# Kernel tuning notes

Measured on AMD Instinct MI355X. Metric: run time of the kernel, lower is better.

Reference implementation:

```python
import jax, jax.numpy as jnp
import numpy as np

N = 50000        # nodes
E = 800000       # edges (before self-loops)
DIM = 96         # model dim
HEADS = 4
HEAD_DIM = DIM // HEADS  # 24
SLOPE = 0.2      # GATConv default negative_slope
EPS = 1e-5       # LayerNorm eps


def setup_inputs() -> dict:
    key = jax.random.key(0)
    ks = jax.random.split(key, 10)
    s = 0.1
    return {
        "x": jax.random.normal(ks[0], (N, DIM), jnp.float32),
        "edge_index": jax.random.randint(ks[1], (2, E), 0, N, dtype=jnp.int64),
        "W": (jax.random.normal(ks[2], (DIM, HEADS * HEAD_DIM), jnp.float32) * s),
        "att_src": (jax.random.normal(ks[3], (HEADS, HEAD_DIM), jnp.float32) * s),
        "att_dst": (jax.random.normal(ks[4], (HEADS, HEAD_DIM), jnp.float32) * s),
        "gat_bias": jnp.zeros((DIM,), jnp.float32),
        "proj_W": (jax.random.normal(ks[5], (DIM, DIM), jnp.float32) * s),
        "proj_b": jnp.zeros((DIM,), jnp.float32),
        "ln_g": jnp.ones((DIM,), jnp.float32),
        "ln_b": jnp.zeros((DIM,), jnp.float32),
    }


def _gat_layer(x, edge_index, W, att_src, att_dst, gat_bias, proj_W, proj_b, ln_g, ln_b):
    # add self-loops (PyG GATConv default add_self_loops=True)
    loop = jnp.arange(N, dtype=edge_index.dtype)
    src = jnp.concatenate([edge_index[0], loop])  # [E+N] message sources j
    dst = jnp.concatenate([edge_index[1], loop])  # [E+N] message targets i

    # shared linear transform, split into heads: [N, H, D]
    h = (x @ W).reshape(N, HEADS, HEAD_DIM)
    a_src = jnp.einsum('nhd,hd->nh', h, att_src)  # [N, H]
    a_dst = jnp.einsum('nhd,hd->nh', h, att_dst)  # [N, H]

    # per-edge attention logits, leaky relu
    e = jax.nn.leaky_relu(a_src[src] + a_dst[dst], SLOPE)  # [E+N, H]

    # segment softmax over incoming edges of each destination node
    m = jax.ops.segment_max(e, dst, num_segments=N)        # [N, H]
    e = jnp.exp(e - m[dst])
    denom = jax.ops.segment_sum(e, dst, num_segments=N)    # [N, H] (>0: self-loops)
    alpha = e / denom[dst]                                 # [E+N, H]

    # weighted scatter-aggregate of source features
    out = jax.ops.segment_sum(alpha[:, :, None] * h[src], dst, num_segments=N)
    out = out.reshape(N, HEADS * HEAD_DIM) + gat_bias      # concat heads + bias

    # trailing proj + residual + LayerNorm (dropout inactive at eval)
    proj = out @ proj_W.T + proj_b
    z = x + proj
    mu = jnp.mean(z, axis=-1, keepdims=True)
    var = jnp.mean((z - mu) ** 2, axis=-1, keepdims=True)
    return ln_g * (z - mu) / jnp.sqrt(var + EPS) + ln_b


def reference(x, edge_index, W, att_src, att_dst, gat_bias, proj_W, proj_b, ln_g, ln_b):
    return _gat_layer(x, edge_index, W, att_src, att_dst, gat_bias, proj_W, proj_b, ln_g, ln_b)
```

## Files before the change

### kernel.cpp

```cpp
#include <hip/hip_runtime.h>
#include <hip/hip_bf16.h>
#include <math.h>

#define N_NODES 50000
#define N_EDGES 800000
#define DIM 96
#define HEADS 4
#define HEAD_DIM 24
#define SLOPE 0.2f
#define LN_EPS 1e-5f

#define CH 2048
#define NCH ((N_EDGES + CH - 1) / CH)
#define NB2 ((N_NODES + 255) / 256)

#define NGRP (N_NODES / 16)
#define GRID_MM 784
#define HLP 100

typedef __attribute__((ext_vector_type(8))) short bf16x8;
typedef __attribute__((ext_vector_type(4))) float f32x4;

__device__ __forceinline__ unsigned short f2bf(float f) {
    unsigned u = __float_as_uint(f);
    u += 0x7FFFu + ((u >> 16) & 1u);
    return (unsigned short)(u >> 16);
}
__device__ __forceinline__ float bf2f(unsigned short v) {
    return __uint_as_float(((unsigned)v) << 16);
}
__device__ __forceinline__ unsigned pack2bf(float a, float b) {
    return (unsigned)f2bf(a) | ((unsigned)f2bf(b) << 16);
}

__global__ __launch_bounds__(256) void k_sortA(
    const int* __restrict__ ei, int* __restrict__ cnt,
    const float* __restrict__ W, const float* __restrict__ PW,
    unsigned short* __restrict__ wfr, unsigned short* __restrict__ pwfr)
{
    const int gi = blockIdx.x * 256 + threadIdx.x;
    if (gi < 2 * 18 * 64) {
        const int a = gi / (18 * 64);
        const int rem = gi % (18 * 64);
        const int frag = rem / 64, lane = rem % 64;
        const int fb = frag / 3, kc = frag % 3;
        const int m = lane & 15, g = lane >> 4;
        unsigned short* dst = (a ? pwfr : wfr) + (size_t)(frag * 64 + lane) * 8;
        #pragma unroll
        for (int j = 0; j < 8; ++j) {
            const int k = kc * 32 + g * 8 + j, f = fb * 16 + m;
            const float v = a ? PW[f * DIM + k] : W[k * DIM + f];
            dst[j] = f2bf(v);
        }
    }
    __shared__ int h[NB2];
    const int b = blockIdx.x, t = threadIdx.x;
    for (int k = t; k < NB2; k += 256) h[k] = 0;
    __syncthreads();
    const int e0 = b * CH;
    const int e1 = (e0 + CH < N_EDGES) ? e0 + CH : N_EDGES;
    for (int e = e0 + t; e < e1; e += 256) {
        const int d = ei[N_EDGES + e];
        if ((unsigned)d < N_NODES) atomicAdd(&h[d >> 8], 1);
    }
    __syncthreads();
    for (int k = t; k < NB2; k += 256) cnt[k * NCH + b] = h[k];
}

__global__ __launch_bounds__(512) void k_sortB1(const int* __restrict__ cnt,
                                                int* __restrict__ colpre,
                                                int* __restrict__ colsum)
{
    __shared__ int s[512];
    const int k = blockIdx.x, t = threadIdx.x;
    const int v = (t < NCH) ? cnt[k * NCH + t] : 0;
    s[t] = v;
    __syncthreads();
    #pragma unroll
    for (int off = 1; off < 512; off <<= 1) {
        const int u = (t >= off) ? s[t - off] : 0;
        __syncthreads();
        s[t] += u;
        __syncthreads();
    }
    if (t < NCH) colpre[k * NCH + t] = s[t] - v;
    if (t == 511) colsum[k] = s[511];
}

__global__ __launch_bounds__(256) void k_sortB2(const int* __restrict__ colsum,
                                                int* __restrict__ bbase)
{
    __shared__ int s[256];
    const int t = threadIdx.x;
    const int v = (t < NB2) ? colsum[t] : 0;
    s[t] = v;
    __syncthreads();
    #pragma unroll
    for (int off = 1; off < 256; off <<= 1) {
        const int u = (t >= off) ? s[t - off] : 0;
        __syncthreads();
        s[t] += u;
        __syncthreads();
    }
    if (t < NB2) bbase[t] = s[t] - v;
    if (t == 255) bbase[NB2] = s[255];
}

__global__ __launch_bounds__(256) void k_sortC(const int* __restrict__ ei,
                                               const int* __restrict__ colpre,
                                               const int* __restrict__ bbase,
                                               unsigned* __restrict__ staged)
{
    __shared__ int lcur[NB2];
    const int b = blockIdx.x, t = threadIdx.x;
    for (int k = t; k < NB2; k += 256) lcur[k] = bbase[k] + colpre[k * NCH + b];
    __syncthreads();
    const int e0 = b * CH;
    const int e1 = (e0 + CH < N_EDGES) ? e0 + CH : N_EDGES;
    for (int e = e0 + t; e < e1; e += 256) {
        int s = ei[e];
        const int d = ei[N_EDGES + e];
        if ((unsigned)d >= N_NODES) continue;
        if ((unsigned)s >= N_NODES) s = d;
        const int pos = atomicAdd(&lcur[d >> 8], 1);
        staged[pos] = (unsigned)s | ((unsigned)(d & 255) << 16);
    }
}

__global__ __launch_bounds__(512) void k_sortD(
    const unsigned* __restrict__ staged, const int* __restrict__ bbase,
    int* __restrict__ offsets, int* __restrict__ ssrc)
{
    __shared__ int hist[256];
    __shared__ int sc[256];
    const int k = blockIdx.x, t = threadIdx.x;
    const int first = k << 8;
    const int nn = (first + 256 < N_NODES) ? 256 : N_NODES - first;
    const int rs = bbase[k], re = bbase[k + 1];
    if (t < 256) hist[t] = 0;
    __syncthreads();
    for (int i = rs + t; i < re; i += 512)
        atomicAdd(&hist[staged[i] >> 16], 1);
    __syncthreads();
    if (t < 256) sc[t] = hist[t];
    __syncthreads();
    #pragma unroll
    for (int off = 1; off < 256; off <<= 1) {
        int u = 0;
        if (t < 256 && t >= off) u = sc[t - off];
        __syncthreads();
        if (t < 256) sc[t] += u;
        __syncthreads();
    }
    int mycur = 0;
    if (t < 256) {
        mycur = rs + sc[t] - hist[t];
        if (t < nn) offsets[first + t] = mycur;
    }
    if (k == 0 && t == 0) offsets[N_NODES] = bbase[NB2];
    __syncthreads();
    if (t < 256) hist[t] = mycur;
    __syncthreads();
    for (int i = rs + t; i < re; i += 512) {
        const unsigned pk = staged[i];
        const int pos = atomicAdd(&hist[pk >> 16], 1);
        ssrc[pos] = (int)(pk & 0xffffu);
    }
}

__global__ __launch_bounds__(256) void k_transform(
    const float* __restrict__ x, const unsigned short* __restrict__ wfr,
    const float* __restrict__ attS, const float* __restrict__ attD,
    unsigned short* __restrict__ hb, float* __restrict__ asrc,
    float* __restrict__ adst)
{
    __shared__ float hl[4][16][HLP];
    const int tid = threadIdx.x, wv = tid >> 6, l = tid & 63;
    const int m = l & 15, g = l >> 4;

    bf16x8 wf[6][3];
    #pragma unroll
    for (int fb = 0; fb < 6; ++fb)
        #pragma unroll
        for (int kc = 0; kc < 3; ++kc)
            wf[fb][kc] = *(const bf16x8*)&wfr[(size_t)((fb * 3 + kc) * 64 + l) * 8];

    float (*h)[HLP] = hl[wv];

    for (int grp = blockIdx.x * 4 + wv; grp < NGRP; grp += gridDim.x * 4) {
        const int n0 = grp * 16;
        f32x4 acc[6];
        #pragma unroll
        for (int fb = 0; fb < 6; ++fb)
            #pragma unroll
            for (int e = 0; e < 4; ++e) acc[fb][e] = 0.f;

        #pragma unroll
        for (int kc = 0; kc < 3; ++kc) {
            const float* xp = x + (size_t)(n0 + m) * DIM + kc * 32 + g * 8;
            const float4 xa = *(const float4*)xp;
            const float4 xb = *(const float4*)(xp + 4);
            uint4 au;
            au.x = pack2bf(xa.x, xa.y); au.y = pack2bf(xa.z, xa.w);
            au.z = pack2bf(xb.x, xb.y); au.w = pack2bf(xb.z, xb.w);
            const bf16x8 af = *(const bf16x8*)&au;
            #pragma unroll
            for (int fb = 0; fb < 6; ++fb)
                acc[fb] = __builtin_amdgcn_mfma_f32_16x16x32_bf16(af, wf[fb][kc], acc[fb], 0, 0, 0);
        }
        #pragma unroll
        for (int fb = 0; fb < 6; ++fb)
            #pragma unroll
            for (int r = 0; r < 4; ++r)
                h[g * 4 + r][fb * 16 + m] = acc[fb][r];

        {
            const int nd = l >> 2, hd = l & 3;
            const float* hr = &h[nd][hd * HEAD_DIM];
            const float* as_ = attS + hd * HEAD_DIM;
            const float* ad_ = attD + hd * HEAD_DIM;
            float s = 0.f, dd = 0.f;
            #pragma unroll
            for (int kk = 0; kk < HEAD_DIM; ++kk) {
                const float hv = hr[kk];
                s += hv * as_[kk];
                dd += hv * ad_[kk];
            }
            asrc[n0 * HEADS + l] = s;
            adst[n0 * HEADS + l] = dd;
        }
        #pragma unroll
        for (int c = l; c < 192; c += 64) {
            const int n = c / 12, q = c % 12;
            const float4 lo = *(const float4*)&h[n][q * 8];
            const float4 hi = *(const float4*)&h[n][q * 8 + 4];
            uint4 hv;
            hv.x = pack2bf(lo.x, lo.y); hv.y = pack2bf(lo.z, lo.w);
            hv.z = pack2bf(hi.x, hi.y); hv.w = pack2bf(hi.z, hi.w);
            *(uint4*)&hb[(size_t)(n0 + n) * DIM + q * 8] = hv;
        }
    }
}

__global__ __launch_bounds__(256) void k_aggregate(
    const int* __restrict__ offsets, const int* __restrict__ ssrc,
    const unsigned short* __restrict__ hb, const float* __restrict__ asrc,
    const float* __restrict__ adst, const float* __restrict__ gb,
    unsigned short* __restrict__ gbuf)
{
    __shared__ float wlds[4][256];
    const int wid  = (blockIdx.x * 256 + threadIdx.x) >> 6;
    const int lane = threadIdx.x & 63;
    if (wid >= N_NODES) return;
    const int wv = (threadIdx.x >> 6) & 3;
    const int d = wid;
    const int lp = (lane < 48) ? lane : 47;
    const int f0 = lp * 2;
    const int hd = f0 / HEAD_DIM;

    const int rs = offsets[d], re = offsets[d + 1];
    const int deg = re - rs;
    const int sv = (lane < deg) ? ssrc[rs + lane] : d;

    {
        const float4 as = *(const float4*)&asrc[sv * 4];
        const float4 ad = *(const float4*)&adst[d * 4];
        float l; float4 w;
        l = as.x + ad.x; l = (l > 0.f) ? l : SLOPE * l; w.x = __expf(l);
        l = as.y + ad.y; l = (l > 0.f) ? l : SLOPE * l; w.y = __expf(l);
        l = as.z + ad.z; l = (l > 0.f) ? l : SLOPE * l; w.z = __expf(l);
        l = as.w + ad.w; l = (l > 0.f) ? l : SLOPE * l; w.w = __expf(l);
        *(float4*)&wlds[wv][lane * 4] = w;
    }

    float acc0, acc1, ds;
    {
        const unsigned hp = *(const unsigned*)&hb[(size_t)d * DIM + f0];
        float l0 = asrc[d * HEADS + hd] + adst[d * HEADS + hd];
        l0 = (l0 > 0.f) ? l0 : SLOPE * l0;
        const float w = __expf(l0);
        acc0 = w * bf2f((unsigned short)(hp & 0xffffu));
        acc1 = w * bf2f((unsigned short)(hp >> 16));
        ds = w;
    }

#define ISSUE(hreg, wreg, j) do { \
        const int s_ = __shfl(sv, (j)); \
        hreg = *(const unsigned*)&hb[(size_t)s_ * DIM + f0]; \
        wreg = wlds[wv][(j) * 4 + hd]; } while (0)
#define CONSUME(hreg, wreg) do { \
        acc0 += (wreg) * bf2f((unsigned short)((hreg) & 0xffffu)); \
        acc1 += (wreg) * bf2f((unsigned short)((hreg) >> 16)); \
        ds += (wreg); } while (0)

    const int nd = (deg < 64) ? deg : 64;
    int j = 0;
    if (nd >= 8) {
        unsigned p0, p1, p2, p3, p4, p5, p6, p7;
        float    q0, q1, q2, q3, q4, q5, q6, q7;
        ISSUE(p0, q0, 0); ISSUE(p1, q1, 1); ISSUE(p2, q2, 2); ISSUE(p3, q3, 3);
        ISSUE(p4, q4, 4); ISSUE(p5, q5, 5); ISSUE(p6, q6, 6); ISSUE(p7, q7, 7);
        for (; j + 16 <= nd; j += 8) {
            CONSUME(p0, q0); ISSUE(p0, q0, j + 8);
            CONSUME(p1, q1); ISSUE(p1, q1, j + 9);
            CONSUME(p2, q2); ISSUE(p2, q2, j + 10);
            CONSUME(p3, q3); ISSUE(p3, q3, j + 11);
            CONSUME(p4, q4); ISSUE(p4, q4, j + 12);
            CONSUME(p5, q5); ISSUE(p5, q5, j + 13);
            CONSUME(p6, q6); ISSUE(p6, q6, j + 14);
            CONSUME(p7, q7); ISSUE(p7, q7, j + 15);
        }
        CONSUME(p0, q0); CONSUME(p1, q1); CONSUME(p2, q2); CONSUME(p3, q3);
        CONSUME(p4, q4); CONSUME(p5, q5); CONSUME(p6, q6); CONSUME(p7, q7);
        j += 8;
    }
    if (j + 4 <= nd) {
        unsigned pa, pb_, pc, pd;
        float    qa, qb, qc, qd;
        ISSUE(pa, qa, j); ISSUE(pb_, qb, j + 1); ISSUE(pc, qc, j + 2); ISSUE(pd, qd, j + 3);
        CONSUME(pa, qa); CONSUME(pb_, qb); CONSUME(pc, qc); CONSUME(pd, qd);
        j += 4;
    }
    for (; j < nd; ++j) {
        unsigned hh; float ww;
        ISSUE(hh, ww, j); CONSUME(hh, ww);
    }
#undef ISSUE
#undef CONSUME
    for (j = 64; j < deg; ++j) {
        const int s_ = ssrc[rs + j];
        const unsigned hh = *(const unsigned*)&hb[(size_t)s_ * DIM + f0];
        float l_ = asrc[s_ * HEADS + hd] + adst[d * HEADS + hd];
        l_ = (l_ > 0.f) ? l_ : SLOPE * l_;
        const float w_ = __expf(l_);
        acc0 += w_ * bf2f((unsigned short)(hh & 0xffffu));
        acc1 += w_ * bf2f((unsigned short)(hh >> 16));
        ds += w_;
    }

    if (lane < 48) {
        const float inv = 1.f / ds;
        const float o0 = acc0 * inv + gb[f0];
        const float o1 = acc1 * inv + gb[f0 + 1];
        *(unsigned*)&gbuf[(size_t)d * DIM + f0] = pack2bf(o0, o1);
    }
}

__global__ __launch_bounds__(256) void k_finalize(
    const float* __restrict__ x, const unsigned short* __restrict__ pwfr,
    const float* __restrict__ pb, const float* __restrict__ lng,
    const float* __restrict__ lnb, const unsigned short* __restrict__ gbuf,
    float* __restrict__ out)
{
    const int tid = threadIdx.x, wv = tid >> 6, l = tid & 63;
    const int m = l & 15, g = l >> 4;

    bf16x8 wf[6][3];
    #pragma unroll
    for (int fb = 0; fb < 6; ++fb)
        #pragma unroll
        for (int kc = 0; kc < 3; ++kc)
            wf[fb][kc] = *(const bf16x8*)&pwfr[(size_t)((fb * 3 + kc) * 64 + l) * 8];

    float pbv[6], lgv[6], lbv[6];
    #pragma unroll
    for (int fb = 0; fb < 6; ++fb) {
        pbv[fb] = pb[fb * 16 + m];
        lgv[fb] = lng[fb * 16 + m];
        lbv[fb] = lnb[fb * 16 + m];
    }

    for (int grp = blockIdx.x * 4 + wv; grp < NGRP; grp += gridDim.x * 4) {
        const int n0 = grp * 16;
        f32x4 acc[6];
        #pragma unroll
        for (int fb = 0; fb < 6; ++fb)
            #pragma unroll
            for (int e = 0; e < 4; ++e) acc[fb][e] = 0.f;

        #pragma unroll
        for (int kc = 0; kc < 3; ++kc) {
            const bf16x8 af = *(const bf16x8*)&gbuf[(size_t)(n0 + m) * DIM + kc * 32 + g * 8];
            #pragma unroll
            for (int fb = 0; fb < 6; ++fb)
                acc[fb] = __builtin_amdgcn_mfma_f32_16x16x32_bf16(af, wf[fb][kc], acc[fb], 0, 0, 0);
        }

        float z[6][4];
        float s0 = 0.f, s1 = 0.f, s2 = 0.f, s3 = 0.f;
        float q0 = 0.f, q1 = 0.f, q2 = 0.f, q3 = 0.f;
        #pragma unroll
        for (int fb = 0; fb < 6; ++fb) {
            #pragma unroll
            for (int r = 0; r < 4; ++r) {
                const float zv = acc[fb][r] + pbv[fb] +
                    x[(size_t)(n0 + g * 4 + r) * DIM + fb * 16 + m];
                z[fb][r] = zv;
                if (r == 0) { s0 += zv; q0 += zv * zv; }
                else if (r == 1) { s1 += zv; q1 += zv * zv; }
                else if (r == 2) { s2 += zv; q2 += zv * zv; }
                else { s3 += zv; q3 += zv * zv; }
            }
        }
        #pragma unroll
        for (int mask = 1; mask < 16; mask <<= 1) {
            s0 += __shfl_xor(s0, mask); q0 += __shfl_xor(q0, mask);
            s1 += __shfl_xor(s1, mask); q1 += __shfl_xor(q1, mask);
            s2 += __shfl_xor(s2, mask); q2 += __shfl_xor(q2, mask);
            s3 += __shfl_xor(s3, mask); q3 += __shfl_xor(q3, mask);
        }
        float mu[4], iv[4];
        mu[0] = s0 * (1.f / DIM); iv[0] = rsqrtf(q0 * (1.f / DIM) - mu[0] * mu[0] + LN_EPS);
        mu[1] = s1 * (1.f / DIM); iv[1] = rsqrtf(q1 * (1.f / DIM) - mu[1] * mu[1] + LN_EPS);
        mu[2] = s2 * (1.f / DIM); iv[2] = rsqrtf(q2 * (1.f / DIM) - mu[2] * mu[2] + LN_EPS);
        mu[3] = s3 * (1.f / DIM); iv[3] = rsqrtf(q3 * (1.f / DIM) - mu[3] * mu[3] + LN_EPS);

        #pragma unroll
        for (int fb = 0; fb < 6; ++fb)
            #pragma unroll
            for (int r = 0; r < 4; ++r)
                out[(size_t)(n0 + g * 4 + r) * DIM + fb * 16 + m] =
                    lgv[fb] * (z[fb][r] - mu[r]) * iv[r] + lbv[fb];
    }
}

extern "C" void kernel_launch(void* const* d_in, const int* in_sizes, int n_in,
                              void* d_out, int out_size, void* d_ws, size_t ws_size,
                              hipStream_t stream)
{
    const float* x    = (const float*)d_in[0];
    const int*   ei   = (const int*)d_in[1];
    const float* W    = (const float*)d_in[2];
    const float* attS = (const float*)d_in[3];
    const float* attD = (const float*)d_in[4];
    const float* gb   = (const float*)d_in[5];
    const float* PW   = (const float*)d_in[6];
    const float* pb   = (const float*)d_in[7];
    const float* lng  = (const float*)d_in[8];
    const float* lnb  = (const float*)d_in[9];
    float* out = (float*)d_out;

    char* ws = (char*)d_ws;
    unsigned* staged = (unsigned*)ws;
    float* asrc    = (float*)(staged + N_EDGES);
    float* adst    = asrc + N_NODES * HEADS;
    unsigned short* hb    = (unsigned short*)(adst + N_NODES * HEADS);
    unsigned short* gbuf  = hb + (size_t)N_NODES * DIM;
    unsigned short* wfrag = gbuf + (size_t)N_NODES * DIM;
    unsigned short* pwfrag= wfrag + 18 * 64 * 8;
    int*   cnt     = (int*)(pwfrag + 18 * 64 * 8);
    int*   colpre  = cnt + NB2 * NCH;
    int*   colsum  = colpre + NB2 * NCH;
    int*   bbase   = colsum + NB2;
    int*   offsets = bbase + NB2 + 1;
    int*   ssrc    = offsets + N_NODES + 1;

    k_sortA    <<<NCH, 256, 0, stream>>>(ei, cnt, W, PW, wfrag, pwfrag);
    k_sortB1   <<<NB2, 512, 0, stream>>>(cnt, colpre, colsum);
    k_sortB2   <<<1, 256, 0, stream>>>(colsum, bbase);
    k_sortC    <<<NCH, 256, 0, stream>>>(ei, colpre, bbase, staged);
    k_sortD    <<<NB2, 512, 0, stream>>>(staged, bbase, offsets, ssrc);
    k_transform<<<GRID_MM, 256, 0, stream>>>(x, wfrag, attS, attD, hb, asrc, adst);
    k_aggregate<<<(N_NODES * 64 + 255) / 256, 256, 0, stream>>>(offsets, ssrc, hb, asrc, adst, gb, gbuf);
    k_finalize <<<GRID_MM, 256, 0, stream>>>(x, pwfrag, pb, lng, lnb, gbuf, out);
}
```

Measured before the change: 87.35 us.

## Process two destination nodes per wavefront and fold bucket scan into sort kernels

The aggregate kernel now assigns two destination nodes to each 64-lane wavefront, overlapping the second node's gather loads with the first node's accumulation and halving the number of waves. The single-block bucket-prefix kernel is removed; each sortC and sortD block redundantly rescans the bucket sums in shared memory, which saves one launch. The trade-off is more registers per thread in aggregate, which may cut occupancy, plus repeated scan work in every sort block. sortD also uses __syncthreads inside divergent branches with matched counts, which is fragile.

```diff
diff --git a/kernel.cpp b/kernel.cpp
--- a/kernel.cpp
+++ b/kernel.cpp
@@ -87,33 +87,25 @@
     if (t == 511) colsum[k] = s[511];
 }
 
-__global__ __launch_bounds__(256) void k_sortB2(const int* __restrict__ colsum,
-                                                int* __restrict__ bbase)
-{
-    __shared__ int s[256];
-    const int t = threadIdx.x;
+__global__ __launch_bounds__(256) void k_sortC(const int* __restrict__ ei,
+                                               const int* __restrict__ colpre,
+                                               const int* __restrict__ colsum,
+                                               unsigned* __restrict__ staged)
+{
+    __shared__ int bs[256];
+    __shared__ int lcur[NB2];
+    const int b = blockIdx.x, t = threadIdx.x;
     const int v = (t < NB2) ? colsum[t] : 0;
-    s[t] = v;
+    bs[t] = v;
     __syncthreads();
     #pragma unroll
     for (int off = 1; off < 256; off <<= 1) {
-        const int u = (t >= off) ? s[t - off] : 0;
-        __syncthreads();
-        s[t] += u;
-        __syncthreads();
-    }
-    if (t < NB2) bbase[t] = s[t] - v;
-    if (t == 255) bbase[NB2] = s[255];
-}
-
-__global__ __launch_bounds__(256) void k_sortC(const int* __restrict__ ei,
-                                               const int* __restrict__ colpre,
-                                               const int* __restrict__ bbase,
-                                               unsigned* __restrict__ staged)
-{
-    __shared__ int lcur[NB2];
-    const int b = blockIdx.x, t = threadIdx.x;
-    for (int k = t; k < NB2; k += 256) lcur[k] = bbase[k] + colpre[k * NCH + b];
+        const int u = (t >= off) ? bs[t - off] : 0;
+        __syncthreads();
+        bs[t] += u;
+        __syncthreads();
+    }
+    if (t < NB2) lcur[t] = (bs[t] - v) + colpre[t * NCH + b];
     __syncthreads();
     const int e0 = b * CH;
     const int e1 = (e0 + CH < N_EDGES) ? e0 + CH : N_EDGES;
@@ -128,15 +120,36 @@
 }
 
 __global__ __launch_bounds__(512) void k_sortD(
-    const unsigned* __restrict__ staged, const int* __restrict__ bbase,
+    const unsigned* __restrict__ staged, const int* __restrict__ colsum,
     int* __restrict__ offsets, int* __restrict__ ssrc)
 {
+    __shared__ int bs[256];
     __shared__ int hist[256];
     __shared__ int sc[256];
+    __shared__ int rs_s, re_s, tot_s;
     const int k = blockIdx.x, t = threadIdx.x;
+    if (t < 256) {
+        const int v = (t < NB2) ? colsum[t] : 0;
+        bs[t] = v;
+        __syncthreads();
+        #pragma unroll
+        for (int off = 1; off < 256; off <<= 1) {
+            const int u = (t >= off) ? bs[t - off] : 0;
+            __syncthreads();
+            bs[t] += u;
+            __syncthreads();
+        }
+        if (t == k) { rs_s = bs[t] - v; re_s = bs[t]; }
+        if (t == NB2 - 1) tot_s = bs[t];
+    } else {
+        __syncthreads();
+        #pragma unroll
+        for (int off = 1; off < 256; off <<= 1) { __syncthreads(); __syncthreads(); }
+    }
+    __syncthreads();
     const int first = k << 8;
     const int nn = (first + 256 < N_NODES) ? 256 : N_NODES - first;
-    const int rs = bbase[k], re = bbase[k + 1];
+    const int rs = rs_s, re = re_s;
     if (t < 256) hist[t] = 0;
     __syncthreads();
     for (int i = rs + t; i < re; i += 512)
@@ -157,7 +170,7 @@
         mycur = rs + sc[t] - hist[t];
         if (t < nn) offsets[first + t] = mycur;
     }
-    if (k == 0 && t == 0) offsets[N_NODES] = bbase[NB2];
+    if (k == 0 && t == 0) offsets[N_NODES] = tot_s;
     __syncthreads();
     if (t < 256) hist[t] = mycur;
     __syncthreads();
@@ -248,101 +261,184 @@
     const float* __restrict__ adst, const float* __restrict__ gb,
     unsigned short* __restrict__ gbuf)
 {
-    __shared__ float wlds[4][256];
+    __shared__ float wlds[4][512];
     const int wid  = (blockIdx.x * 256 + threadIdx.x) >> 6;
     const int lane = threadIdx.x & 63;
-    if (wid >= N_NODES) return;
+    const int d0 = wid * 2;
+    if (d0 >= N_NODES) return;
+    const int d1 = d0 + 1;
     const int wv = (threadIdx.x >> 6) & 3;
-    const int d = wid;
     const int lp = (lane < 48) ? lane : 47;
     const int f0 = lp * 2;
     const int hd = f0 / HEAD_DIM;
 
-    const int rs = offsets[d], re = offsets[d + 1];
-    const int deg = re - rs;
-    const int sv = (lane < deg) ? ssrc[rs + lane] : d;
+    const int rs0 = offsets[d0], re0 = offsets[d1], re1 = offsets[d0 + 2];
+    const int deg0 = re0 - rs0, deg1 = re1 - re0;
+
+    const int sv0 = (lane < deg0) ? ssrc[rs0 + lane] : d0;
+    const int sv1 = (lane < deg1) ? ssrc[re0 + lane] : d1;
 
     {
-        const float4 as = *(const float4*)&asrc[sv * 4];
-        const float4 ad = *(const float4*)&adst[d * 4];
+        const float4 as0 = *(const float4*)&asrc[sv0 * 4];
+        const float4 ad0 = *(const float4*)&adst[d0 * 4];
+        const float4 as1 = *(const float4*)&asrc[sv1 * 4];
+        const float4 ad1 = *(const float4*)&adst[d1 * 4];
         float l; float4 w;
-        l = as.x + ad.x; l = (l > 0.f) ? l : SLOPE * l; w.x = __expf(l);
-        l = as.y + ad.y; l = (l > 0.f) ? l : SLOPE * l; w.y = __expf(l);
-        l = as.z + ad.z; l = (l > 0.f) ? l : SLOPE * l; w.z = __expf(l);
-        l = as.w + ad.w; l = (l > 0.f) ? l : SLOPE * l; w.w = __expf(l);
+        l = as0.x + ad0.x; l = (l > 0.f) ? l : SLOPE * l; w.x = __expf(l);
+        l = as0.y + ad0.y; l = (l > 0.f) ? l : SLOPE * l; w.y = __expf(l);
+        l = as0.z + ad0.z; l = (l > 0.f) ? l : SLOPE * l; w.z = __expf(l);
+        l = as0.w + ad0.w; l = (l > 0.f) ? l : SLOPE * l; w.w = __expf(l);
         *(float4*)&wlds[wv][lane * 4] = w;
-    }
-
-    float acc0, acc1, ds;
+        l = as1.x + ad1.x; l = (l > 0.f) ? l : SLOPE * l; w.x = __expf(l);
+        l = as1.y + ad1.y; l = (l > 0.f) ? l : SLOPE * l; w.y = __expf(l);
+        l = as1.z + ad1.z; l = (l > 0.f) ? l : SLOPE * l; w.z = __expf(l);
+        l = as1.w + ad1.w; l = (l > 0.f) ? l : SLOPE * l; w.w = __expf(l);
+        *(float4*)&wlds[wv][(64 + lane) * 4] = w;
+    }
+
+    float a00, a01, ds0, a10, a11, ds1;
     {
-        const unsigned hp = *(const unsigned*)&hb[(size_t)d * DIM + f0];
-        float l0 = asrc[d * HEADS + hd] + adst[d * HEADS + hd];
+        const unsigned hp0 = *(const unsigned*)&hb[(size_t)d0 * DIM + f0];
+        const unsigned hp1 = *(const unsigned*)&hb[(size_t)d1 * DIM + f0];
+        float l0 = asrc[d0 * HEADS + hd] + adst[d0 * HEADS + hd];
         l0 = (l0 > 0.f) ? l0 : SLOPE * l0;
-        const float w = __expf(l0);
-        acc0 = w * bf2f((unsigned short)(hp & 0xffffu));
-        acc1 = w * bf2f((unsigned short)(hp >> 16));
-        ds = w;
-    }
-
-#define ISSUE(hreg, wreg, j) do { \
-        const int s_ = __shfl(sv, (j)); \
+        const float w0 = __expf(l0);
+        a00 = w0 * bf2f((unsigned short)(hp0 & 0xffffu));
+        a01 = w0 * bf2f((unsigned short)(hp0 >> 16));
+        ds0 = w0;
+        float l1 = asrc[d1 * HEADS + hd] + adst[d1 * HEADS + hd];
+        l1 = (l1 > 0.f) ? l1 : SLOPE * l1;
+        const float w1 = __expf(l1);
+        a10 = w1 * bf2f((unsigned short)(hp1 & 0xffffu));
+        a11 = w1 * bf2f((unsigned short)(hp1 >> 16));
+        ds1 = w1;
+    }
+
+#define ISSUE(hreg, wreg, svv, base, j) do { \
+        const int s_ = __shfl(svv, (j)); \
         hreg = *(const unsigned*)&hb[(size_t)s_ * DIM + f0]; \
-        wreg = wlds[wv][(j) * 4 + hd]; } while (0)
-#define CONSUME(hreg, wreg) do { \
-        acc0 += (wreg) * bf2f((unsigned short)((hreg) & 0xffffu)); \
-        acc1 += (wreg) * bf2f((unsigned short)((hreg) >> 16)); \
-        ds += (wreg); } while (0)
-
-    const int nd = (deg < 64) ? deg : 64;
-    int j = 0;
-    if (nd >= 8) {
+        wreg = wlds[wv][((base) + (j)) * 4 + hd]; } while (0)
+#define CONS(hreg, wreg, A0, A1, DS) do { \
+        A0 += (wreg) * bf2f((unsigned short)((hreg) & 0xffffu)); \
+        A1 += (wreg) * bf2f((unsigned short)((hreg) >> 16)); \
+        DS += (wreg); } while (0)
+
+    const int nd0 = (deg0 < 64) ? deg0 : 64;
+    const int nd1 = (deg1 < 64) ? deg1 : 64;
+    unsigned B0, B1, B2, B3, B4, B5, B6, B7;
+    float    u0, u1, u2, u3, u4, u5, u6, u7;
+    bool bfilled = false;
+
+    int ja = 0;
+    if (nd0 >= 8) {
         unsigned p0, p1, p2, p3, p4, p5, p6, p7;
         float    q0, q1, q2, q3, q4, q5, q6, q7;
-        ISSUE(p0, q0, 0); ISSUE(p1, q1, 1); ISSUE(p2, q2, 2); ISSUE(p3, q3, 3);
-        ISSUE(p4, q4, 4); ISSUE(p5, q5, 5); ISSUE(p6, q6, 6); ISSUE(p7, q7, 7);
-        for (; j + 16 <= nd; j += 8) {
-            CONSUME(p0, q0); ISSUE(p0, q0, j + 8);
-            CONSUME(p1, q1); ISSUE(p1, q1, j + 9);
-            CONSUME(p2, q2); ISSUE(p2, q2, j + 10);
-            CONSUME(p3, q3); ISSUE(p3, q3, j + 11);
-            CONSUME(p4, q4); ISSUE(p4, q4, j + 12);
-            CONSUME(p5, q5); ISSUE(p5, q5, j + 13);
-            CONSUME(p6, q6); ISSUE(p6, q6, j + 14);
-            CONSUME(p7, q7); ISSUE(p7, q7, j + 15);
-        }
-        CONSUME(p0, q0); CONSUME(p1, q1); CONSUME(p2, q2); CONSUME(p3, q3);
-        CONSUME(p4, q4); CONSUME(p5, q5); CONSUME(p6, q6); CONSUME(p7, q7);
-        j += 8;
-    }
-    if (j + 4 <= nd) {
+        ISSUE(p0, q0, sv0, 0, 0); ISSUE(p1, q1, sv0, 0, 1);
+        ISSUE(p2, q2, sv0, 0, 2); ISSUE(p3, q3, sv0, 0, 3);
+        ISSUE(p4, q4, sv0, 0, 4); ISSUE(p5, q5, sv0, 0, 5);
+        ISSUE(p6, q6, sv0, 0, 6); ISSUE(p7, q7, sv0, 0, 7);
+        for (; ja + 16 <= nd0; ja += 8) {
+            CONS(p0, q0, a00, a01, ds0); ISSUE(p0, q0, sv0, 0, ja + 8);
+            CONS(p1, q1, a00, a01, ds0); ISSUE(p1, q1, sv0, 0, ja + 9);
+            CONS(p2, q2, a00, a01, ds0); ISSUE(p2, q2, sv0, 0, ja + 10);
+            CONS(p3, q3, a00, a01, ds0); ISSUE(p3, q3, sv0, 0, ja + 11);
+            CONS(p4, q4, a00, a01, ds0); ISSUE(p4, q4, sv0, 0, ja + 12);
+            CONS(p5, q5, a00, a01, ds0); ISSUE(p5, q5, sv0, 0, ja + 13);
+            CONS(p6, q6, a00, a01, ds0); ISSUE(p6, q6, sv0, 0, ja + 14);
+            CONS(p7, q7, a00, a01, ds0); ISSUE(p7, q7, sv0, 0, ja + 15);
+        }
+        if (nd1 >= 8) {
+            ISSUE(B0, u0, sv1, 64, 0); ISSUE(B1, u1, sv1, 64, 1);
+            ISSUE(B2, u2, sv1, 64, 2); ISSUE(B3, u3, sv1, 64, 3);
+            ISSUE(B4, u4, sv1, 64, 4); ISSUE(B5, u5, sv1, 64, 5);
+            ISSUE(B6, u6, sv1, 64, 6); ISSUE(B7, u7, sv1, 64, 7);
+            bfilled = true;
+        }
+        CONS(p0, q0, a00, a01, ds0); CONS(p1, q1, a00, a01, ds0);
+        CONS(p2, q2, a00, a01, ds0); CONS(p3, q3, a00, a01, ds0);
+        CONS(p4, q4, a00, a01, ds0); CONS(p5, q5, a00, a01, ds0);
+        CONS(p6, q6, a00, a01, ds0); CONS(p7, q7, a00, a01, ds0);
+        ja += 8;
+    } else if (nd1 >= 8) {
+        ISSUE(B0, u0, sv1, 64, 0); ISSUE(B1, u1, sv1, 64, 1);
+        ISSUE(B2, u2, sv1, 64, 2); ISSUE(B3, u3, sv1, 64, 3);
+        ISSUE(B4, u4, sv1, 64, 4); ISSUE(B5, u5, sv1, 64, 5);
+        ISSUE(B6, u6, sv1, 64, 6); ISSUE(B7, u7, sv1, 64, 7);
+        bfilled = true;
+    }
+    if (ja + 4 <= nd0) {
         unsigned pa, pb_, pc, pd;
         float    qa, qb, qc, qd;
-        ISSUE(pa, qa, j); ISSUE(pb_, qb, j + 1); ISSUE(pc, qc, j + 2); ISSUE(pd, qd, j + 3);
-        CONSUME(pa, qa); CONSUME(pb_, qb); CONSUME(pc, qc); CONSUME(pd, qd);
-        j += 4;
-    }
-    for (; j < nd; ++j) {
+        ISSUE(pa, qa, sv0, 0, ja);     ISSUE(pb_, qb, sv0, 0, ja + 1);
+        ISSUE(pc, qc, sv0, 0, ja + 2); ISSUE(pd, qd, sv0, 0, ja + 3);
+        CONS(pa, qa, a00, a01, ds0); CONS(pb_, qb, a00, a01, ds0);
+        CONS(pc, qc, a00, a01, ds0); CONS(pd, qd, a00, a01, ds0);
+        ja += 4;
+    }
+    for (; ja < nd0; ++ja) {
         unsigned hh; float ww;
-        ISSUE(hh, ww, j); CONSUME(hh, ww);
+        ISSUE(hh, ww, sv0, 0, ja); CONS(hh, ww, a00, a01, ds0);
+    }
+
+    int jb = 0;
+    if (bfilled) {
+        for (; jb + 16 <= nd1; jb += 8) {
+            CONS(B0, u0, a10, a11, ds1); ISSUE(B0, u0, sv1, 64, jb + 8);
+            CONS(B1, u1, a10, a11, ds1); ISSUE(B1, u1, sv1, 64, jb + 9);
+            CONS(B2, u2, a10, a11, ds1); ISSUE(B2, u2, sv1, 64, jb + 10);
+            CONS(B3, u3, a10, a11, ds1); ISSUE(B3, u3, sv1, 64, jb + 11);
+            CONS(B4, u4, a10, a11, ds1); ISSUE(B4, u4, sv1, 64, jb + 12);
+            CONS(B5, u5, a10, a11, ds1); ISSUE(B5, u5, sv1, 64, jb + 13);
+            CONS(B6, u6, a10, a11, ds1); ISSUE(B6, u6, sv1, 64, jb + 14);
+            CONS(B7, u7, a10, a11, ds1); ISSUE(B7, u7, sv1, 64, jb + 15);
+        }
+        CONS(B0, u0, a10, a11, ds1); CONS(B1, u1, a10, a11, ds1);
+        CONS(B2, u2, a10, a11, ds1); CONS(B3, u3, a10, a11, ds1);
+        CONS(B4, u4, a10, a11, ds1); CONS(B5, u5, a10, a11, ds1);
+        CONS(B6, u6, a10, a11, ds1); CONS(B7, u7, a10, a11, ds1);
+        jb += 8;
+    }
+    if (jb + 4 <= nd1) {
+        unsigned pa, pb_, pc, pd;
+        float    qa, qb, qc, qd;
+        ISSUE(pa, qa, sv1, 64, jb);     ISSUE(pb_, qb, sv1, 64, jb + 1);
+        ISSUE(pc, qc, sv1, 64, jb + 2); ISSUE(pd, qd, sv1, 64, jb + 3);
+        CONS(pa, qa, a10, a11, ds1); CONS(pb_, qb, a10, a11, ds1);
+        CONS(pc, qc, a10, a11, ds1); CONS(pd, qd, a10, a11, ds1);
+        jb += 4;
+    }
+    for (; jb < nd1; ++jb) {
+        unsigned hh; float ww;
+        ISSUE(hh, ww, sv1, 64, jb); CONS(hh, ww, a10, a11, ds1);
     }
 #undef ISSUE
-#undef CONSUME
-    for (j = 64; j < deg; ++j) {
-        const int s_ = ssrc[rs + j];
+#undef CONS
+    for (int j = 64; j < deg0; ++j) {
+        const int s_ = ssrc[rs0 + j];
         const unsigned hh = *(const unsigned*)&hb[(size_t)s_ * DIM + f0];
-        float l_ = asrc[s_ * HEADS + hd] + adst[d * HEADS + hd];
+        float l_ = asrc[s_ * HEADS + hd] + adst[d0 * HEADS + hd];
         l_ = (l_ > 0.f) ? l_ : SLOPE * l_;
         const float w_ = __expf(l_);
-        acc0 += w_ * bf2f((unsigned short)(hh & 0xffffu));
-        acc1 += w_ * bf2f((unsigned short)(hh >> 16));
-        ds += w_;
+        a00 += w_ * bf2f((unsigned short)(hh & 0xffffu));
+        a01 += w_ * bf2f((unsigned short)(hh >> 16));
+        ds0 += w_;
+    }
+    for (int j = 64; j < deg1; ++j) {
+        const int s_ = ssrc[re0 + j];
+        const unsigned hh = *(const unsigned*)&hb[(size_t)s_ * DIM + f0];
+        float l_ = asrc[s_ * HEADS + hd] + adst[d1 * HEADS + hd];
+        l_ = (l_ > 0.f) ? l_ : SLOPE * l_;
+        const float w_ = __expf(l_);
+        a10 += w_ * bf2f((unsigned short)(hh & 0xffffu));
+        a11 += w_ * bf2f((unsigned short)(hh >> 16));
+        ds1 += w_;
     }
 
     if (lane < 48) {
-        const float inv = 1.f / ds;
-        const float o0 = acc0 * inv + gb[f0];
-        const float o1 = acc1 * inv + gb[f0 + 1];
-        *(unsigned*)&gbuf[(size_t)d * DIM + f0] = pack2bf(o0, o1);
+        const float i0 = 1.f / ds0, i1 = 1.f / ds1;
+        const float g0 = gb[f0], g1 = gb[f0 + 1];
+        *(unsigned*)&gbuf[(size_t)d0 * DIM + f0] = pack2bf(a00 * i0 + g0, a01 * i0 + g1);
+        *(unsigned*)&gbuf[(size_t)d1 * DIM + f0] = pack2bf(a10 * i1 + g0, a11 * i1 + g1);
     }
 }
 
@@ -451,16 +547,14 @@
     int*   cnt     = (int*)(pwfrag + 18 * 64 * 8);
     int*   colpre  = cnt + NB2 * NCH;
     int*   colsum  = colpre + NB2 * NCH;
-    int*   bbase   = colsum + NB2;
-    int*   offsets = bbase + NB2 + 1;
+    int*   offsets = colsum + NB2;
     int*   ssrc    = offsets + N_NODES + 1;
 
     k_sortA    <<<NCH, 256, 0, stream>>>(ei, cnt, W, PW, wfrag, pwfrag);
     k_sortB1   <<<NB2, 512, 0, stream>>>(cnt, colpre, colsum);
-    k_sortB2   <<<1, 256, 0, stream>>>(colsum, bbase);
-    k_sortC    <<<NCH, 256, 0, stream>>>(ei, colpre, bbase, staged);
-    k_sortD    <<<NB2, 512, 0, stream>>>(staged, bbase, offsets, ssrc);
+    k_sortC    <<<NCH, 256, 0, stream>>>(ei, colpre, colsum, staged);
+    k_sortD    <<<NB2, 512, 0, stream>>>(staged, colsum, offsets, ssrc);
     k_transform<<<GRID_MM, 256, 0, stream>>>(x, wfrag, attS, attD, hb, asrc, adst);
-    k_aggregate<<<(N_NODES * 64 + 255) / 256, 256, 0, stream>>>(offsets, ssrc, hb, asrc, adst, gb, gbuf);
+    k_aggregate<<<(N_NODES / 2 * 64 + 255) / 256, 256, 0, stream>>>(offsets, ssrc, hb, asrc, adst, gb, gbuf);
     k_finalize <<<GRID_MM, 256, 0, stream>>>(x, pwfrag, pb, lng, lnb, gbuf, out);
 }
```

Measured after the change: 88.83 us. About the same (+1.7%).

## Fuse aggregation with projection+LayerNorm and fold bucket prefix scan into sort kernels

Applied to the files above, without the earlier changes.

Merges the aggregation and finalize kernels, so each block aggregates 16 nodes into a shared-memory bf16 tile and one wave then runs the MFMA projection, residual and LayerNorm. This removes the gbuf round trip through global memory and one launch. It also deletes the single-block bucket scan kernel by redoing the small colsum prefix scan inside sortC and sortD, which removes another launch. The cost is that three of the four waves sit idle during the epilogue, the projection weights are reloaded per block, and every sort block now repeats the scan.

```diff
diff --git a/kernel.cpp b/kernel.cpp
--- a/kernel.cpp
+++ b/kernel.cpp
@@ -17,6 +17,7 @@
 #define NGRP (N_NODES / 16)
 #define GRID_MM 784
 #define HLP 100
+#define GTP 104
 
 typedef __attribute__((ext_vector_type(8))) short bf16x8;
 typedef __attribute__((ext_vector_type(4))) float f32x4;
@@ -87,33 +88,25 @@
     if (t == 511) colsum[k] = s[511];
 }
 
-__global__ __launch_bounds__(256) void k_sortB2(const int* __restrict__ colsum,
-                                                int* __restrict__ bbase)
-{
-    __shared__ int s[256];
-    const int t = threadIdx.x;
-    const int v = (t < NB2) ? colsum[t] : 0;
-    s[t] = v;
-    __syncthreads();
-    #pragma unroll
-    for (int off = 1; off < 256; off <<= 1) {
-        const int u = (t >= off) ? s[t - off] : 0;
-        __syncthreads();
-        s[t] += u;
-        __syncthreads();
-    }
-    if (t < NB2) bbase[t] = s[t] - v;
-    if (t == 255) bbase[NB2] = s[255];
-}
-
 __global__ __launch_bounds__(256) void k_sortC(const int* __restrict__ ei,
                                                const int* __restrict__ colpre,
-                                               const int* __restrict__ bbase,
+                                               const int* __restrict__ colsum,
                                                unsigned* __restrict__ staged)
 {
+    __shared__ int bs[256];
     __shared__ int lcur[NB2];
     const int b = blockIdx.x, t = threadIdx.x;
-    for (int k = t; k < NB2; k += 256) lcur[k] = bbase[k] + colpre[k * NCH + b];
+    const int v = (t < NB2) ? colsum[t] : 0;
+    bs[t] = v;
+    __syncthreads();
+    #pragma unroll
+    for (int off = 1; off < 256; off <<= 1) {
+        const int u = (t >= off) ? bs[t - off] : 0;
+        __syncthreads();
+        bs[t] += u;
+        __syncthreads();
+    }
+    if (t < NB2) lcur[t] = (bs[t] - v) + colpre[t * NCH + b];
     __syncthreads();
     const int e0 = b * CH;
     const int e1 = (e0 + CH < N_EDGES) ? e0 + CH : N_EDGES;
@@ -128,15 +121,36 @@
 }
 
 __global__ __launch_bounds__(512) void k_sortD(
-    const unsigned* __restrict__ staged, const int* __restrict__ bbase,
+    const unsigned* __restrict__ staged, const int* __restrict__ colsum,
     int* __restrict__ offsets, int* __restrict__ ssrc)
 {
+    __shared__ int bs[256];
     __shared__ int hist[256];
     __shared__ int sc[256];
+    __shared__ int rs_s, re_s, tot_s;
     const int k = blockIdx.x, t = threadIdx.x;
+    if (t < 256) {
+        const int v = (t < NB2) ? colsum[t] : 0;
+        bs[t] = v;
+        __syncthreads();
+        #pragma unroll
+        for (int off = 1; off < 256; off <<= 1) {
+            const int u = (t >= off) ? bs[t - off] : 0;
+            __syncthreads();
+            bs[t] += u;
+            __syncthreads();
+        }
+        if (t == k) { rs_s = bs[t] - v; re_s = bs[t]; }
+        if (t == NB2 - 1) tot_s = bs[t];
+    } else {
+        __syncthreads();
+        #pragma unroll
+        for (int off = 1; off < 256; off <<= 1) { __syncthreads(); __syncthreads(); }
+    }
+    __syncthreads();
     const int first = k << 8;
     const int nn = (first + 256 < N_NODES) ? 256 : N_NODES - first;
-    const int rs = bbase[k], re = bbase[k + 1];
+    const int rs = rs_s, re = re_s;
     if (t < 256) hist[t] = 0;
     __syncthreads();
     for (int i = rs + t; i < re; i += 512)
@@ -157,7 +171,7 @@
         mycur = rs + sc[t] - hist[t];
         if (t < nn) offsets[first + t] = mycur;
     }
-    if (k == 0 && t == 0) offsets[N_NODES] = bbase[NB2];
+    if (k == 0 && t == 0) offsets[N_NODES] = tot_s;
     __syncthreads();
     if (t < 256) hist[t] = mycur;
     __syncthreads();
@@ -242,47 +256,50 @@
     }
 }
 
-__global__ __launch_bounds__(256) void k_aggregate(
+__global__ __launch_bounds__(256) void k_aggfin(
     const int* __restrict__ offsets, const int* __restrict__ ssrc,
     const unsigned short* __restrict__ hb, const float* __restrict__ asrc,
     const float* __restrict__ adst, const float* __restrict__ gb,
-    unsigned short* __restrict__ gbuf)
+    const unsigned short* __restrict__ pwfr, const float* __restrict__ x,
+    const float* __restrict__ pb, const float* __restrict__ lng,
+    const float* __restrict__ lnb, float* __restrict__ out)
 {
     __shared__ float wlds[4][256];
-    const int wid  = (blockIdx.x * 256 + threadIdx.x) >> 6;
-    const int lane = threadIdx.x & 63;
-    if (wid >= N_NODES) return;
-    const int wv = (threadIdx.x >> 6) & 3;
-    const int d = wid;
+    __shared__ unsigned short gtile[16][GTP];
+    const int tid = threadIdx.x, wv = tid >> 6, lane = tid & 63;
+    const int n0 = blockIdx.x * 16;
     const int lp = (lane < 48) ? lane : 47;
     const int f0 = lp * 2;
     const int hd = f0 / HEAD_DIM;
-
-    const int rs = offsets[d], re = offsets[d + 1];
-    const int deg = re - rs;
-    const int sv = (lane < deg) ? ssrc[rs + lane] : d;
-
-    {
-        const float4 as = *(const float4*)&asrc[sv * 4];
-        const float4 ad = *(const float4*)&adst[d * 4];
-        float l; float4 w;
-        l = as.x + ad.x; l = (l > 0.f) ? l : SLOPE * l; w.x = __expf(l);
-        l = as.y + ad.y; l = (l > 0.f) ? l : SLOPE * l; w.y = __expf(l);
-        l = as.z + ad.z; l = (l > 0.f) ? l : SLOPE * l; w.z = __expf(l);
-        l = as.w + ad.w; l = (l > 0.f) ? l : SLOPE * l; w.w = __expf(l);
-        *(float4*)&wlds[wv][lane * 4] = w;
-    }
-
-    float acc0, acc1, ds;
-    {
-        const unsigned hp = *(const unsigned*)&hb[(size_t)d * DIM + f0];
-        float l0 = asrc[d * HEADS + hd] + adst[d * HEADS + hd];
-        l0 = (l0 > 0.f) ? l0 : SLOPE * l0;
-        const float w = __expf(l0);
-        acc0 = w * bf2f((unsigned short)(hp & 0xffffu));
-        acc1 = w * bf2f((unsigned short)(hp >> 16));
-        ds = w;
-    }
+    const float gb0 = gb[f0], gb1 = gb[f0 + 1];
+
+    for (int i = 0; i < 4; ++i) {
+        const int d = n0 + wv * 4 + i;
+        const int rs = offsets[d], re = offsets[d + 1];
+        const int deg = re - rs;
+        const int sv = (lane < deg) ? ssrc[rs + lane] : d;
+
+        {
+            const float4 as = *(const float4*)&asrc[sv * 4];
+            const float4 ad = *(const float4*)&adst[d * 4];
+            float l; float4 w;
+            l = as.x + ad.x; l = (l > 0.f) ? l : SLOPE * l; w.x = __expf(l);
+            l = as.y + ad.y; l = (l > 0.f) ? l : SLOPE * l; w.y = __expf(l);
+            l = as.z + ad.z; l = (l > 0.f) ? l : SLOPE * l; w.z = __expf(l);
+            l = as.w + ad.w; l = (l > 0.f) ? l : SLOPE * l; w.w = __expf(l);
+            *(float4*)&wlds[wv][lane * 4] = w;
+        }
+
+        float acc0, acc1, ds;
+        {
+            const unsigned hp = *(const unsigned*)&hb[(size_t)d * DIM + f0];
+            float l0 = asrc[d * HEADS + hd] + adst[d * HEADS + hd];
+            l0 = (l0 > 0.f) ? l0 : SLOPE * l0;
+            const float w = __expf(l0);
+            acc0 = w * bf2f((unsigned short)(hp & 0xffffu));
+            acc1 = w * bf2f((unsigned short)(hp >> 16));
+            ds = w;
+        }
 
 #define ISSUE(hreg, wreg, j) do { \
         const int s_ = __shfl(sv, (j)); \
@@ -293,134 +310,114 @@
         acc1 += (wreg) * bf2f((unsigned short)((hreg) >> 16)); \
         ds += (wreg); } while (0)
 
-    const int nd = (deg < 64) ? deg : 64;
-    int j = 0;
-    if (nd >= 8) {
-        unsigned p0, p1, p2, p3, p4, p5, p6, p7;
-        float    q0, q1, q2, q3, q4, q5, q6, q7;
-        ISSUE(p0, q0, 0); ISSUE(p1, q1, 1); ISSUE(p2, q2, 2); ISSUE(p3, q3, 3);
-        ISSUE(p4, q4, 4); ISSUE(p5, q5, 5); ISSUE(p6, q6, 6); ISSUE(p7, q7, 7);
-        for (; j + 16 <= nd; j += 8) {
-            CONSUME(p0, q0); ISSUE(p0, q0, j + 8);
-            CONSUME(p1, q1); ISSUE(p1, q1, j + 9);
-            CONSUME(p2, q2); ISSUE(p2, q2, j + 10);
-            CONSUME(p3, q3); ISSUE(p3, q3, j + 11);
-            CONSUME(p4, q4); ISSUE(p4, q4, j + 12);
-            CONSUME(p5, q5); ISSUE(p5, q5, j + 13);
-            CONSUME(p6, q6); ISSUE(p6, q6, j + 14);
-            CONSUME(p7, q7); ISSUE(p7, q7, j + 15);
-        }
-        CONSUME(p0, q0); CONSUME(p1, q1); CONSUME(p2, q2); CONSUME(p3, q3);
-        CONSUME(p4, q4); CONSUME(p5, q5); CONSUME(p6, q6); CONSUME(p7, q7);
-        j += 8;
-    }
-    if (j + 4 <= nd) {
-        unsigned pa, pb_, pc, pd;
-        float    qa, qb, qc, qd;
-        ISSUE(pa, qa, j); ISSUE(pb_, qb, j + 1); ISSUE(pc, qc, j + 2); ISSUE(pd, qd, j + 3);
-        CONSUME(pa, qa); CONSUME(pb_, qb); CONSUME(pc, qc); CONSUME(pd, qd);
-        j += 4;
-    }
-    for (; j < nd; ++j) {
-        unsigned hh; float ww;
-        ISSUE(hh, ww, j); CONSUME(hh, ww);
-    }
+        const int nd = (deg < 64) ? deg : 64;
+        int j = 0;
+        if (nd >= 8) {
+            unsigned p0, p1, p2, p3, p4, p5, p6, p7;
+            float    q0, q1, q2, q3, q4, q5, q6, q7;
+            ISSUE(p0, q0, 0); ISSUE(p1, q1, 1); ISSUE(p2, q2, 2); ISSUE(p3, q3, 3);
+            ISSUE(p4, q4, 4); ISSUE(p5, q5, 5); ISSUE(p6, q6, 6); ISSUE(p7, q7, 7);
+            for (; j + 16 <= nd; j += 8) {
+                CONSUME(p0, q0); ISSUE(p0, q0, j + 8);
+                CONSUME(p1, q1); ISSUE(p1, q1, j + 9);
+                CONSUME(p2, q2); ISSUE(p2, q2, j + 10);
+                CONSUME(p3, q3); ISSUE(p3, q3, j + 11);
+                CONSUME(p4, q4); ISSUE(p4, q4, j + 12);
+                CONSUME(p5, q5); ISSUE(p5, q5, j + 13);
+                CONSUME(p6, q6); ISSUE(p6, q6, j + 14);
+                CONSUME(p7, q7); ISSUE(p7, q7, j + 15);
+            }
+            CONSUME(p0, q0); CONSUME(p1, q1); CONSUME(p2, q2); CONSUME(p3, q3);
+            CONSUME(p4, q4); CONSUME(p5, q5); CONSUME(p6, q6); CONSUME(p7, q7);
+            j += 8;
+        }
+        if (j + 4 <= nd) {
+            unsigned pa, pb_, pc, pd;
+            float    qa, qb, qc, qd;
+            ISSUE(pa, qa, j); ISSUE(pb_, qb, j + 1); ISSUE(pc, qc, j + 2); ISSUE(pd, qd, j + 3);
+            CONSUME(pa, qa); CONSUME(pb_, qb); CONSUME(pc, qc); CONSUME(pd, qd);
+            j += 4;
+        }
+        for (; j < nd; ++j) {
+            unsigned hh; float ww;
+            ISSUE(hh, ww, j); CONSUME(hh, ww);
+        }
 #undef ISSUE
 #undef CONSUME
-    for (j = 64; j < deg; ++j) {
-        const int s_ = ssrc[rs + j];
-        const unsigned hh = *(const unsigned*)&hb[(size_t)s_ * DIM + f0];
-        float l_ = asrc[s_ * HEADS + hd] + adst[d * HEADS + hd];
-        l_ = (l_ > 0.f) ? l_ : SLOPE * l_;
-        const float w_ = __expf(l_);
-        acc0 += w_ * bf2f((unsigned short)(hh & 0xffffu));
-        acc1 += w_ * bf2f((unsigned short)(hh >> 16));
-        ds += w_;
-    }
-
-    if (lane < 48) {
-        const float inv = 1.f / ds;
-        const float o0 = acc0 * inv + gb[f0];
-        const float o1 = acc1 * inv + gb[f0 + 1];
-        *(unsigned*)&gbuf[(size_t)d * DIM + f0] = pack2bf(o0, o1);
-    }
-}
-
-__global__ __launch_bounds__(256) void k_finalize(
-    const float* __restrict__ x, const unsigned short* __restrict__ pwfr,
-    const float* __restrict__ pb, const float* __restrict__ lng,
-    const float* __restrict__ lnb, const unsigned short* __restrict__ gbuf,
-    float* __restrict__ out)
-{
-    const int tid = threadIdx.x, wv = tid >> 6, l = tid & 63;
-    const int m = l & 15, g = l >> 4;
-
-    bf16x8 wf[6][3];
+        for (j = 64; j < deg; ++j) {
+            const int s_ = ssrc[rs + j];
+            const unsigned hh = *(const unsigned*)&hb[(size_t)s_ * DIM + f0];
+            float l_ = asrc[s_ * HEADS + hd] + adst[d * HEADS + hd];
+            l_ = (l_ > 0.f) ? l_ : SLOPE * l_;
+            const float w_ = __expf(l_);
+            acc0 += w_ * bf2f((unsigned short)(hh & 0xffffu));
+            acc1 += w_ * bf2f((unsigned short)(hh >> 16));
+            ds += w_;
+        }
+
+        if (lane < 48) {
+            const float inv = 1.f / ds;
+            *(unsigned*)&gtile[wv * 4 + i][f0] =
+                pack2bf(acc0 * inv + gb0, acc1 * inv + gb1);
+        }
+    }
+    __syncthreads();
+    if (wv != 0) return;
+
+    const int m = lane & 15, g2 = lane >> 4;
+    f32x4 acc[6];
     #pragma unroll
     for (int fb = 0; fb < 6; ++fb)
         #pragma unroll
-        for (int kc = 0; kc < 3; ++kc)
-            wf[fb][kc] = *(const bf16x8*)&pwfr[(size_t)((fb * 3 + kc) * 64 + l) * 8];
-
-    float pbv[6], lgv[6], lbv[6];
+        for (int e = 0; e < 4; ++e) acc[fb][e] = 0.f;
+
+    #pragma unroll
+    for (int kc = 0; kc < 3; ++kc) {
+        const bf16x8 af = *(const bf16x8*)&gtile[m][kc * 32 + g2 * 8];
+        #pragma unroll
+        for (int fb = 0; fb < 6; ++fb) {
+            const bf16x8 bf_ = *(const bf16x8*)&pwfr[(size_t)((fb * 3 + kc) * 64 + lane) * 8];
+            acc[fb] = __builtin_amdgcn_mfma_f32_16x16x32_bf16(af, bf_, acc[fb], 0, 0, 0);
+        }
+    }
+
+    float z[6][4];
+    float s0 = 0.f, s1 = 0.f, s2 = 0.f, s3 = 0.f;
+    float q0 = 0.f, q1 = 0.f, q2 = 0.f, q3 = 0.f;
     #pragma unroll
     for (int fb = 0; fb < 6; ++fb) {
-        pbv[fb] = pb[fb * 16 + m];
-        lgv[fb] = lng[fb * 16 + m];
-        lbv[fb] = lnb[fb * 16 + m];
-    }
-
-    for (int grp = blockIdx.x * 4 + wv; grp < NGRP; grp += gridDim.x * 4) {
-        const int n0 = grp * 16;
-        f32x4 acc[6];
-        #pragma unroll
-        for (int fb = 0; fb < 6; ++fb)
-            #pragma unroll
-            for (int e = 0; e < 4; ++e) acc[fb][e] = 0.f;
-
-        #pragma unroll
-        for (int kc = 0; kc < 3; ++kc) {
-            const bf16x8 af = *(const bf16x8*)&gbuf[(size_t)(n0 + m) * DIM + kc * 32 + g * 8];
-            #pragma unroll
-            for (int fb = 0; fb < 6; ++fb)
-                acc[fb] = __builtin_amdgcn_mfma_f32_16x16x32_bf16(af, wf[fb][kc], acc[fb], 0, 0, 0);
-        }
-
-        float z[6][4];
-        float s0 = 0.f, s1 = 0.f, s2 = 0.f, s3 = 0.f;
-        float q0 = 0.f, q1 = 0.f, q2 = 0.f, q3 = 0.f;
-        #pragma unroll
-        for (int fb = 0; fb < 6; ++fb) {
-            #pragma unroll
-            for (int r = 0; r < 4; ++r) {
-                const float zv = acc[fb][r] + pbv[fb] +
-                    x[(size_t)(n0 + g * 4 + r) * DIM + fb * 16 + m];
-                z[fb][r] = zv;
-                if (r == 0) { s0 += zv; q0 += zv * zv; }
-                else if (r == 1) { s1 += zv; q1 += zv * zv; }
-                else if (r == 2) { s2 += zv; q2 += zv * zv; }
-                else { s3 += zv; q3 += zv * zv; }
-            }
-        }
-        #pragma unroll
-        for (int mask = 1; mask < 16; mask <<= 1) {
-            s0 += __shfl_xor(s0, mask); q0 += __shfl_xor(q0, mask);
-            s1 += __shfl_xor(s1, mask); q1 += __shfl_xor(q1, mask);
-            s2 += __shfl_xor(s2, mask); q2 += __shfl_xor(q2, mask);
-            s3 += __shfl_xor(s3, mask); q3 += __shfl_xor(q3, mask);
-        }
-        float mu[4], iv[4];
-        mu[0] = s0 * (1.f / DIM); iv[0] = rsqrtf(q0 * (1.f / DIM) - mu[0] * mu[0] + LN_EPS);
-        mu[1] = s1 * (1.f / DIM); iv[1] = rsqrtf(q1 * (1.f / DIM) - mu[1] * mu[1] + LN_EPS);
-        mu[2] = s2 * (1.f / DIM); iv[2] = rsqrtf(q2 * (1.f / DIM) - mu[2] * mu[2] + LN_EPS);
-        mu[3] = s3 * (1.f / DIM); iv[3] = rsqrtf(q3 * (1.f / DIM) - mu[3] * mu[3] + LN_EPS);
-
-        #pragma unroll
-        for (int fb = 0; fb < 6; ++fb)
-            #pragma unroll
-            for (int r = 0; r < 4; ++r)
-                out[(size_t)(n0 + g * 4 + r) * DIM + fb * 16 + m] =
-                    lgv[fb] * (z[fb][r] - mu[r]) * iv[r] + lbv[fb];
+        const float pbv = pb[fb * 16 + m];
+        #pragma unroll
+        for (int r = 0; r < 4; ++r) {
+            const float zv = acc[fb][r] + pbv +
+                x[(size_t)(n0 + g2 * 4 + r) * DIM + fb * 16 + m];
+            z[fb][r] = zv;
+            if (r == 0) { s0 += zv; q0 += zv * zv; }
+            else if (r == 1) { s1 += zv; q1 += zv * zv; }
+            else if (r == 2) { s2 += zv; q2 += zv * zv; }
+            else { s3 += zv; q3 += zv * zv; }
+        }
+    }
+    #pragma unroll
+    for (int mask = 1; mask < 16; mask <<= 1) {
+        s0 += __shfl_xor(s0, mask); q0 += __shfl_xor(q0, mask);
+        s1 += __shfl_xor(s1, mask); q1 += __shfl_xor(q1, mask);
+        s2 += __shfl_xor(s2, mask); q2 += __shfl_xor(q2, mask);
+        s3 += __shfl_xor(s3, mask); q3 += __shfl_xor(q3, mask);
+    }
+    float mu[4], iv[4];
+    mu[0] = s0 * (1.f / DIM); iv[0] = rsqrtf(q0 * (1.f / DIM) - mu[0] * mu[0] + LN_EPS);
+    mu[1] = s1 * (1.f / DIM); iv[1] = rsqrtf(q1 * (1.f / DIM) - mu[1] * mu[1] + LN_EPS);
+    mu[2] = s2 * (1.f / DIM); iv[2] = rsqrtf(q2 * (1.f / DIM) - mu[2] * mu[2] + LN_EPS);
+    mu[3] = s3 * (1.f / DIM); iv[3] = rsqrtf(q3 * (1.f / DIM) - mu[3] * mu[3] + LN_EPS);
+
+    #pragma unroll
+    for (int fb = 0; fb < 6; ++fb) {
+        const float lgv = lng[fb * 16 + m], lbv = lnb[fb * 16 + m];
+        #pragma unroll
+        for (int r = 0; r < 4; ++r)
+            out[(size_t)(n0 + g2 * 4 + r) * DIM + fb * 16 + m] =
+                lgv * (z[fb][r] - mu[r]) * iv[r] + lbv;
     }
 }
 
@@ -445,22 +442,19 @@
     float* asrc    = (float*)(staged + N_EDGES);
     float* adst    = asrc + N_NODES * HEADS;
     unsigned short* hb    = (unsigned short*)(adst + N_NODES * HEADS);
-    unsigned short* gbuf  = hb + (size_t)N_NODES * DIM;
-    unsigned short* wfrag = gbuf + (size_t)N_NODES * DIM;
+    unsigned short* wfrag = hb + (size_t)N_NODES * DIM;
     unsigned short* pwfrag= wfrag + 18 * 64 * 8;
     int*   cnt     = (int*)(pwfrag + 18 * 64 * 8);
     int*   colpre  = cnt + NB2 * NCH;
     int*   colsum  = colpre + NB2 * NCH;
-    int*   bbase   = colsum + NB2;
-    int*   offsets = bbase + NB2 + 1;
+    int*   offsets = colsum + NB2;
     int*   ssrc    = offsets + N_NODES + 1;
 
     k_sortA    <<<NCH, 256, 0, stream>>>(ei, cnt, W, PW, wfrag, pwfrag);
     k_sortB1   <<<NB2, 512, 0, stream>>>(cnt, colpre, colsum);
-    k_sortB2   <<<1, 256, 0, stream>>>(colsum, bbase);
-    k_sortC    <<<NCH, 256, 0, stream>>>(ei, colpre, bbase, staged);
-    k_sortD    <<<NB2, 512, 0, stream>>>(staged, bbase, offsets, ssrc);
+    k_sortC    <<<NCH, 256, 0, stream>>>(ei, colpre, colsum, staged);
+    k_sortD    <<<NB2, 512, 0, stream>>>(staged, colsum, offsets, ssrc);
     k_transform<<<GRID_MM, 256, 0, stream>>>(x, wfrag, attS, attD, hb, asrc, adst);
-    k_aggregate<<<(N_NODES * 64 + 255) / 256, 256, 0, stream>>>(offsets, ssrc, hb, asrc, adst, gb, gbuf);
-    k_finalize <<<GRID_MM, 256, 0, stream>>>(x, pwfrag, pb, lng, lnb, gbuf, out);
-}
+    k_aggfin   <<<NGRP, 256, 0, stream>>>(offsets, ssrc, hb, asrc, adst, gb,
+                                          pwfrag, x, pb, lng, lnb, out);
+}
```

Result: slower. 111.9 us (+28.1%).
